# Performance work log

Measured on AMD Instinct MI355X. Metric: run time of the kernel, lower is better.

## Reference

```python
import jax, jax.numpy as jnp
import numpy as np

CHANNELS = 1024
N_HEADS = 16
N_EMBD = 512
H_DIM = CHANNELS // N_HEADS


def setup_inputs() -> dict:
    key = jax.random.key(0)
    ks = jax.random.split(key, 10)
    b, hw = 16, 4096
    s = 0.02
    return {
        "x": jax.random.normal(ks[0], (b, hw, CHANNELS), dtype=jnp.float32),
        "p": jax.random.normal(ks[1], (b, 77, N_EMBD), dtype=jnp.float32),
        "Wq": jax.random.normal(ks[2], (CHANNELS, CHANNELS), dtype=jnp.float32) * s,
        "bq": jnp.zeros((CHANNELS,), dtype=jnp.float32),
        "Wk": jax.random.normal(ks[3], (N_EMBD, CHANNELS), dtype=jnp.float32) * s,
        "bk": jnp.zeros((CHANNELS,), dtype=jnp.float32),
        "Wv": jax.random.normal(ks[4], (N_EMBD, CHANNELS), dtype=jnp.float32) * s,
        "bv": jnp.zeros((CHANNELS,), dtype=jnp.float32),
        "Ww": jax.random.normal(ks[5], (CHANNELS, CHANNELS), dtype=jnp.float32) * s,
        "bw": jnp.zeros((CHANNELS,), dtype=jnp.float32),
    }


def reference(x, p, Wq, bq, Wk, bk, Wv, bv, Ww, bw):
    b, hw, c = x.shape
    # Linear projections (torch Linear: y = x @ W^T + b; here weights stored as (in, out))
    q = x @ Wq + bq                      # (b, hw, c)
    k = p @ Wk + bk                      # (b, 77, c)
    v = p @ Wv + bv                      # (b, 77, c)
    q = q.reshape(b, hw, N_HEADS, H_DIM)
    k = k.reshape(b, 77, N_HEADS, H_DIM)
    v = v.reshape(b, 77, N_HEADS, H_DIM)
    scale = 1.0 / jnp.sqrt(jnp.asarray(H_DIM, dtype=x.dtype))
    # scores: (b, heads, hw, 77)
    scores = jnp.einsum("bqhd,bkhd->bhqk", q, k) * scale
    attn = jax.nn.softmax(scores, axis=-1)
    out = jnp.einsum("bhqk,bkhd->bqhd", attn, v).reshape(b, hw, c)
    return out @ Ww + bw
```

## Files before the change

kernel.cpp:

```cpp
#include <hip/hip_runtime.h>
#include <cstdint>
#include <type_traits>

typedef uint16_t u16;
typedef uint32_t u32;
typedef __attribute__((ext_vector_type(4))) float f32x4;
typedef __attribute__((ext_vector_type(8))) __bf16 vbf8;
typedef __attribute__((ext_vector_type(8))) short vs8;

template <typename T, typename = void>
struct CanMfma : std::false_type {};
template <typename T>
struct CanMfma<T, std::void_t<decltype(__builtin_amdgcn_mfma_f32_16x16x32_bf16(
    std::declval<T>(), std::declval<T>(), std::declval<f32x4>(), 0, 0, 0))>>
    : std::true_type {};
typedef std::conditional_t<CanMfma<vbf8>::value, vbf8, vs8> frag_t;

__device__ __forceinline__ f32x4 mfma_bf16(frag_t a, frag_t b, f32x4 c) {
  return __builtin_amdgcn_mfma_f32_16x16x32_bf16(a, b, c, 0, 0, 0);
}

__device__ __forceinline__ u16 f2bf(float f) {
  u32 u = __builtin_bit_cast(u32, f);
  u32 r = (u + 0x7FFFu + ((u >> 16) & 1u)) >> 16;
  return (u16)r;
}

__device__ __forceinline__ void gload_lds16(const void* g, void* l) {
  __builtin_amdgcn_global_load_lds(
      (const __attribute__((address_space(1))) void*)g,
      (__attribute__((address_space(3))) void*)l, 16, 0, 0);
}

__device__ __forceinline__ void transpose_body(
    const float* __restrict__ in, u16* __restrict__ out, int K, int N,
    int k0, int n0, float (*tile)[33]) {
  const int tr = threadIdx.x >> 5, tc = threadIdx.x & 31;
#pragma unroll
  for (int i = 0; i < 4; ++i)
    tile[tr + i * 8][tc] = in[(size_t)(k0 + tr + i * 8) * N + (n0 + tc)];
  __syncthreads();
#pragma unroll
  for (int i = 0; i < 4; ++i)
    out[(size_t)(n0 + tr + i * 8) * K + (k0 + tc)] = f2bf(tile[tc][tr + i * 8]);
}

__global__ __launch_bounds__(256) void prep_kernel(
    const float* __restrict__ x, const float* __restrict__ p,
    const float* __restrict__ Wq, const float* __restrict__ Ww,
    const float* __restrict__ Wk, const float* __restrict__ Wv,
    u16* __restrict__ x_bf, u16* __restrict__ p_bf,
    u16* __restrict__ wq_t, u16* __restrict__ ww_t, u16* __restrict__ wkv_t) {
  __shared__ float tile[32][33];
  const int bid = blockIdx.x;
  if (bid < 32768) {
    const size_t i = (size_t)bid * 256 + threadIdx.x;
    const float4 a  = ((const float4*)x)[i * 2];
    const float4 b2 = ((const float4*)x)[i * 2 + 1];
    uint4 o;
    o.x = (u32)f2bf(a.x)  | ((u32)f2bf(a.y)  << 16);
    o.y = (u32)f2bf(a.z)  | ((u32)f2bf(a.w)  << 16);
    o.z = (u32)f2bf(b2.x) | ((u32)f2bf(b2.y) << 16);
    o.w = (u32)f2bf(b2.z) | ((u32)f2bf(b2.w) << 16);
    ((uint4*)x_bf)[i] = o;
  } else if (bid < 33076) {
    const int i = (bid - 32768) * 256 + threadIdx.x;
    if (i < 78848) {
      const float4 a  = ((const float4*)p)[(size_t)i * 2];
      const float4 b2 = ((const float4*)p)[(size_t)i * 2 + 1];
      uint4 o;
      o.x = (u32)f2bf(a.x)  | ((u32)f2bf(a.y)  << 16);
      o.y = (u32)f2bf(a.z)  | ((u32)f2bf(a.w)  << 16);
      o.z = (u32)f2bf(b2.x) | ((u32)f2bf(b2.y) << 16);
      o.w = (u32)f2bf(b2.z) | ((u32)f2bf(b2.w) << 16);
      ((uint4*)p_bf)[(size_t)i] = o;
    }
  } else if (bid < 35124) {
    const bool isQ = bid < 34100;
    const int r = (bid - (isQ ? 33076 : 34100));
    transpose_body(isQ ? Wq : Ww, isQ ? wq_t : ww_t, 1024, 1024,
                   (r & 31) * 32, (r >> 5) * 32, tile);
  } else {
    const bool isK = bid < 35636;
    const int r = (bid - (isK ? 35124 : 35636));
    transpose_body(isK ? Wk : Wv, isK ? wkv_t : (wkv_t + 1024 * 512), 512, 1024,
                   (r & 15) * 32, (r >> 4) * 32, tile);
  }
}

template <bool OUT_BF16>
__global__ __launch_bounds__(256) void gemm_bt(
    const u16* __restrict__ A, const u16* __restrict__ Bt,
    const float* __restrict__ biasA, const float* __restrict__ biasB,
    void* __restrict__ Cout,
    int M, int N, int K, int Mtiles, int Ntiles) {
  __shared__ char Al[2][128 * 32 * 2];
  __shared__ char Bl[2][128 * 32 * 2];

  const int nwg = Mtiles * Ntiles;
  int bid = (int)blockIdx.x;
  bid = (bid & 7) * (nwg >> 3) + (bid >> 3);
  const int mt = bid / Ntiles, nt = bid % Ntiles;
  const int m0 = mt * 128, n0 = nt * 128;

  const int tid = (int)threadIdx.x;
  const int lane = tid & 63;
  const int wv = tid >> 6;
  const int wm = wv & 1, wn = wv >> 1;
  const int lr = lane & 15, lg = lane >> 4;
  const int rsub = lane >> 2;
  const int slot = lane & 3;
  const int rb0 = n0 + rsub;

  auto stage = [&](int buf, int t) {
    const int k0 = t << 5;
#pragma unroll
    for (int c = 0; c < 2; ++c) {
      const int ci = c * 4 + wv;
      int rra = m0 + ci * 16 + rsub;
      if (rra >= M) rra = M - 1;
      gload_lds16(A + (size_t)rra * K + k0 + slot * 8, Al[buf] + ci * 1024);
      const int rrb = rb0 + ci * 16;
      gload_lds16(Bt + (size_t)rrb * K + k0 + slot * 8, Bl[buf] + ci * 1024);
    }
  };

  f32x4 zero4 = {0.f, 0.f, 0.f, 0.f};
  f32x4 acc[4][4];
#pragma unroll
  for (int i = 0; i < 4; ++i)
#pragma unroll
    for (int j = 0; j < 4; ++j) acc[i][j] = zero4;

  const int nk = K >> 5;
  int cur = 0;
  stage(0, 0);
  __syncthreads();

  for (int t = 0; t < nk; ++t) {
    if (t + 1 < nk) stage(cur ^ 1, t + 1);
    frag_t af[4], bf[4];
#pragma unroll
    for (int i = 0; i < 4; ++i) {
      af[i] = *(const frag_t*)(Al[cur] + (wm * 64 + i * 16 + lr) * 64 + lg * 16);
      bf[i] = *(const frag_t*)(Bl[cur] + (wn * 64 + i * 16 + lr) * 64 + lg * 16);
    }
#pragma unroll
    for (int i = 0; i < 4; ++i)
#pragma unroll
      for (int j = 0; j < 4; ++j)
        acc[i][j] = mfma_bf16(af[i], bf[j], acc[i][j]);
    __syncthreads();
    cur ^= 1;
  }

#pragma unroll
  for (int j = 0; j < 4; ++j) {
    const int col = n0 + wn * 64 + j * 16 + lr;
    const float bv = (col < 1024) ? biasA[col] : biasB[col - 1024];
#pragma unroll
    for (int i = 0; i < 4; ++i) {
      const int rbase = m0 + wm * 64 + i * 16 + lg * 4;
#pragma unroll
      for (int r = 0; r < 4; ++r) {
        const int row = rbase + r;
        const float val = acc[i][j][r] + bv;
        if constexpr (OUT_BF16) {
          u32 me = f2bf(val);
          u32 other = __shfl_xor(me, 1);
          if ((lane & 1) == 0 && row < M) {
            *(u32*)((u16*)Cout + (size_t)row * N + col) = me | (other << 16);
          }
        } else {
          if (row < M) ((float*)Cout)[(size_t)row * N + col] = val;
        }
      }
    }
  }
}

template <bool OUT_BF16>
__global__ __launch_bounds__(512, 4) void gemm256(
    const u16* __restrict__ A, const u16* __restrict__ Bt,
    const float* __restrict__ bias, void* __restrict__ Cout,
    int M, int N, int K) {
  __shared__ u16 Al[2][256 * 32];
  __shared__ u16 Bl[2][128 * 32];

  const int Ntiles = N >> 7;
  const int nwg = (M >> 8) * Ntiles;
  int bid = (int)blockIdx.x;
  bid = (bid & 7) * (nwg >> 3) + (bid >> 3);
  const int mt = bid / Ntiles, ntl = bid % Ntiles;
  const int m0 = mt << 8, n0 = ntl << 7;

  const int tid = (int)threadIdx.x;
  const int lane = tid & 63;
  const int wid = tid >> 6;
  const int wm = wid >> 1, wn = wid & 1;
  const int lr = lane & 15, lg = lane >> 4;

  const int srow = lane >> 2;
  const int sslot = (lane & 3) ^ ((lane >> 3) & 3);
  const u16* Abase = A + (size_t)(m0 + wid * 32 + srow) * K + sslot * 8;
  const u16* Bbase = Bt + (size_t)(n0 + wid * 16 + srow) * K + sslot * 8;

  auto stage = [&](u16* da, u16* db, int t) {
    const int k0 = t << 5;
    gload_lds16(Abase + k0, (char*)da + wid * 2048);
    gload_lds16(Abase + ((size_t)K << 4) + k0, (char*)da + wid * 2048 + 1024);
    gload_lds16(Bbase + k0, (char*)db + wid * 1024);
  };

  auto ldsF = [&](const u16* base, int row) -> frag_t {
    const int phys = lg ^ ((row >> 1) & 3);
    return *(const frag_t*)(base + (size_t)row * 32 + phys * 8);
  };

  f32x4 zero4 = {0.f, 0.f, 0.f, 0.f};
  f32x4 acc[4][4];
#pragma unroll
  for (int i = 0; i < 4; ++i)
#pragma unroll
    for (int j = 0; j < 4; ++j) acc[i][j] = zero4;

  const int nt = K >> 5;
  const int ar0 = wm * 64 + lr;
  const int br0 = wn * 64 + lr;

  stage(&Al[0][0], &Bl[0][0], 0);
  stage(&Al[1][0], &Bl[1][0], 1);
  asm volatile("s_waitcnt vmcnt(3)" ::: "memory");
  __builtin_amdgcn_s_barrier();

  for (int t = 0; t < nt; ++t) {
    const int cur = t & 1;
    const u16* al = &Al[cur][0];
    const u16* bl = &Bl[cur][0];
    if (t >= 1 && t + 1 < nt)
      stage(&Al[cur ^ 1][0], &Bl[cur ^ 1][0], t + 1);
    frag_t a[4], b[4];
#pragma unroll
    for (int i = 0; i < 4; ++i) a[i] = ldsF(al, ar0 + i * 16);
#pragma unroll
    for (int j = 0; j < 4; ++j) b[j] = ldsF(bl, br0 + j * 16);
#pragma unroll
    for (int i = 0; i < 4; ++i)
#pragma unroll
      for (int j = 0; j < 4; ++j)
        acc[i][j] = mfma_bf16(a[i], b[j], acc[i][j]);
    if (t + 1 < nt) {
      asm volatile("s_waitcnt vmcnt(0)" ::: "memory");
      __builtin_amdgcn_s_barrier();
    }
  }

  float bvv[4];
#pragma unroll
  for (int bj = 0; bj < 4; ++bj) bvv[bj] = bias[n0 + wn * 64 + bj * 16 + lr];
#pragma unroll
  for (int ai = 0; ai < 4; ++ai) {
    const int rbase = m0 + wm * 64 + ai * 16 + lg * 4;
#pragma unroll
    for (int rr = 0; rr < 4; ++rr) {
      const int row = rbase + rr;
#pragma unroll
      for (int bj = 0; bj < 4; ++bj) {
        const int cb = n0 + wn * 64 + bj * 16;
        const float val = acc[ai][bj][rr] + bvv[bj];
        if constexpr (OUT_BF16) {
          u32 me = f2bf(val);
          u32 d0 = me | (__shfl_xor(me, 1) << 16);
          u32 d1 = __shfl_xor(d0, 2);
          if ((lane & 3) == 0) {
            uint2 o; o.x = d0; o.y = d1;
            *(uint2*)((u16*)Cout + (size_t)row * N + cb + (lr & 12)) = o;
          }
        } else {
          float v0 = val;
          float v1 = __shfl_xor(v0, 1);
          float v2 = __shfl_xor(v0, 2);
          float v3 = __shfl_xor(v1, 2);
          if ((lane & 3) == 0) {
            float4 o; o.x = v0; o.y = v1; o.z = v2; o.w = v3;
            *(float4*)((float*)Cout + (size_t)row * N + cb + (lr & 12)) = o;
          }
        }
      }
    }
  }
}

__global__ __launch_bounds__(256) void attn_kernel(
    const u16* __restrict__ Q, const u16* __restrict__ KV,
    u16* __restrict__ O) {
  __shared__ u16 Kl[96][72];
  __shared__ u16 Vt[64][104];

  const int bid = blockIdx.x;
  const int qt0 = bid & 15;
  const int h = (bid >> 4) & 15;
  const int b = bid >> 8;
  const int tid = threadIdx.x;

#pragma unroll
  for (int it = 0; it < 3; ++it) {
    const int idx = tid + it * 256;
    const int key = idx >> 3, s = idx & 7;
    uint4 val{0u, 0u, 0u, 0u};
    if (key < 77)
      val = *(const uint4*)(KV + ((size_t)(b * 77 + key)) * 2048 + h * 64 + s * 8);
    *(uint4*)(&Kl[key][s * 8]) = val;
  }
#pragma unroll
  for (int it = 0; it < 3; ++it) {
    const int idx = tid + it * 256;
    if (idx < 616) {
      const int key = idx >> 3, s = idx & 7;
      const uint4 v4 = *(const uint4*)(KV + ((size_t)(b * 77 + key)) * 2048 +
                                       1024 + h * 64 + s * 8);
      const u16* e = (const u16*)&v4;
#pragma unroll
      for (int j = 0; j < 8; ++j) Vt[s * 8 + j][key] = e[j];
    }
  }
#pragma unroll
  for (int it = 0; it < 5; ++it) {
    const int idx = tid + it * 256;
    if (idx < 1216) {
      const int d = idx / 19, kk = 77 + idx % 19;
      Vt[d][kk] = 0;
    }
  }
  __syncthreads();

  const int lane = tid & 63;
  const int wv = tid >> 6;
  const int lr = lane & 15;
  const int lg = lane >> 4;
  f32x4 zero4 = {0.f, 0.f, 0.f, 0.f};

  for (int q4 = 0; q4 < 4; ++q4) {
    const int qt = qt0 * 4 + q4;

    const size_t qrow = (size_t)(b * 4096 + qt * 64 + wv * 16 + lr) * 1024 + h * 64;
    frag_t qf[2];
#pragma unroll
    for (int ks = 0; ks < 2; ++ks)
      qf[ks] = *(const frag_t*)(Q + qrow + ks * 32 + lg * 8);

    f32x4 sa[5] = {zero4, zero4, zero4, zero4, zero4};
#pragma unroll
    for (int ks = 0; ks < 2; ++ks) {
#pragma unroll
      for (int kt = 0; kt < 5; ++kt) {
        frag_t kf = *(const frag_t*)(&Kl[kt * 16 + lr][ks * 32 + lg * 8]);
        sa[kt] = mfma_bf16(kf, qf[ks], sa[kt]);
      }
    }

    float p[5][4];
    float mx = -3.0e38f;
#pragma unroll
    for (int kt = 0; kt < 5; ++kt)
#pragma unroll
      for (int r = 0; r < 4; ++r) {
        const int key = kt * 16 + lg * 4 + r;
        float s = sa[kt][r] * 0.125f;
        if (key >= 77) s = -3.0e38f;
        p[kt][r] = s;
        mx = fmaxf(mx, s);
      }
    mx = fmaxf(mx, __shfl_xor(mx, 16));
    mx = fmaxf(mx, __shfl_xor(mx, 32));
    float sum = 0.f;
#pragma unroll
    for (int kt = 0; kt < 5; ++kt)
#pragma unroll
      for (int r = 0; r < 4; ++r) {
        const float e = __expf(p[kt][r] - mx);
        p[kt][r] = e;
        sum += e;
      }
    sum += __shfl_xor(sum, 16);
    sum += __shfl_xor(sum, 32);
    const float rden = 1.0f / sum;
#pragma unroll
    for (int kt = 0; kt < 5; ++kt)
#pragma unroll
      for (int r = 0; r < 4; ++r) p[kt][r] *= rden;

    union FP { frag_t v; u16 e[8]; };
    frag_t pa[3];
#pragma unroll
    for (int kb = 0; kb < 3; ++kb) {
      FP f;
#pragma unroll
      for (int j = 0; j < 8; ++j) {
        const int kt = 2 * kb + (j >> 2);
        f.e[j] = (kt < 5) ? f2bf(p[kt][j & 3]) : (u16)0;
      }
      pa[kb] = f.v;
    }

    f32x4 oa[4] = {zero4, zero4, zero4, zero4};
#pragma unroll
    for (int nt = 0; nt < 4; ++nt) {
      const int d = nt * 16 + lr;
#pragma unroll
      for (int kb = 0; kb < 3; ++kb) {
        const int key0 = kb * 32 + lg * 4;
        FP vb;
        *(uint2*)(&vb.e[0]) = *(const uint2*)(&Vt[d][key0]);
        *(uint2*)(&vb.e[4]) = *(const uint2*)(&Vt[d][key0 + 16]);
        oa[nt] = mfma_bf16(pa[kb], vb.v, oa[nt]);
      }
    }

#pragma unroll
    for (int nt = 0; nt < 4; ++nt)
#pragma unroll
      for (int r = 0; r < 4; ++r) {
        const int qr = wv * 16 + lg * 4 + r;
        u32 me = f2bf(oa[nt][r]);
        u32 other = __shfl_xor(me, 1);
        if ((lane & 1) == 0) {
          *(u32*)(O + ((size_t)(b * 4096 + qt * 64 + qr)) * 1024 + h * 64 +
                  nt * 16 + lr) = me | (other << 16);
        }
      }
  }
}

extern "C" void kernel_launch(void* const* d_in, const int* in_sizes, int n_in,
                              void* d_out, int out_size, void* d_ws, size_t ws_size,
                              hipStream_t stream) {
  const float* x  = (const float*)d_in[0];
  const float* p  = (const float*)d_in[1];
  const float* Wq = (const float*)d_in[2];
  const float* bq = (const float*)d_in[3];
  const float* Wk = (const float*)d_in[4];
  const float* bk = (const float*)d_in[5];
  const float* Wv = (const float*)d_in[6];
  const float* bv = (const float*)d_in[7];
  const float* Ww = (const float*)d_in[8];
  const float* bw = (const float*)d_in[9];

  char* ws = (char*)d_ws;
  if (ws_size < 281034752ULL) return;

  u16* x_bf  = (u16*)(ws + 0);
  u16* q_bf  = (u16*)(ws + 134217728);
  u16* wq_t  = (u16*)(ws + 268435456);
  u16* ww_t  = (u16*)(ws + 270532608);
  u16* wkv_t = (u16*)(ws + 272629760);
  u16* p_bf  = (u16*)(ws + 274726912);
  u16* kv_bf = (u16*)(ws + 275988480);

  prep_kernel<<<36148, 256, 0, stream>>>(x, p, Wq, Ww, Wk, Wv,
                                         x_bf, p_bf, wq_t, ww_t, wkv_t);
  gemm_bt<true><<<160, 256, 0, stream>>>(p_bf, wkv_t, bk, bv, kv_bf,
                                         1232, 2048, 512, 10, 16);
  gemm256<true><<<2048, 512, 0, stream>>>(x_bf, wq_t, bq, q_bf, 65536, 1024, 1024);
  attn_kernel<<<4096, 256, 0, stream>>>(q_bf, kv_bf, x_bf);
  gemm256<false><<<2048, 512, 0, stream>>>(x_bf, ww_t, bw, d_out, 65536, 1024, 1024);
}
```

Baseline: 589.3 us.

## Add 256x256-tile ping-pong pipelined GEMM for the Q projection

Adds a new gemm8p kernel using 256x256 output tiles with 8 waves, double-buffered LDS filled by direct global-to-LDS loads, and a fine-grained schedule. That schedule interleaves LDS fragment reads, next-tile staging and MFMA quarters, using barriers, sched_barrier and setprio. It replaces gemm256 only for the Q projection, halving the grid to 1024 blocks. The aim is to hide global and LDS latency behind MFMA work and raise data reuse per tile. The trade-off is high register pressure from 128 accumulators at one block per CU, plus reliance on hand-tuned waitcnt counts.

```diff
diff --git a/kernel.cpp b/kernel.cpp
--- a/kernel.cpp
+++ b/kernel.cpp
@@ -31,6 +31,8 @@
       (const __attribute__((address_space(1))) void*)g,
       (__attribute__((address_space(3))) void*)l, 16, 0, 0);
 }
+
+#define SB0() __builtin_amdgcn_sched_barrier(0)
 
 __device__ __forceinline__ void transpose_body(
     const float* __restrict__ in, u16* __restrict__ out, int K, int N,
@@ -291,6 +293,183 @@
   }
 }
 
+template <bool OUT_BF16>
+__global__ __launch_bounds__(512, 1) void gemm8p(
+    const u16* __restrict__ A, const u16* __restrict__ Bt,
+    const float* __restrict__ bias, void* __restrict__ Cout,
+    int M, int N, int K) {
+  __shared__ u16 Al[2][256 * 64];
+  __shared__ u16 Bl[2][256 * 64];
+
+  const int Ntiles = N >> 8;
+  const int nwg = (M >> 8) * Ntiles;
+  int bid = (int)blockIdx.x;
+  bid = (bid & 7) * (nwg >> 3) + (bid >> 3);
+  const int mt = bid / Ntiles, ntl = bid % Ntiles;
+  const int m0 = mt << 8, n0 = ntl << 8;
+
+  const int tid = (int)threadIdx.x;
+  const int lane = tid & 63;
+  const int wid = tid >> 6;
+  const int wm = wid >> 2, wn = wid & 3;
+  const int lr = lane & 15, lg = lane >> 4;
+  const int sslot = (lane & 7) ^ (lane >> 3);
+  const int lrow = lane >> 3;
+
+  auto stageA = [&](u16* dst, int half, int t) {
+#pragma unroll
+    for (int sub = 0; sub < 2; ++sub) {
+      const int s = half + sub * 2;
+      const u16* g = A + (size_t)(m0 + s * 64 + wid * 8 + lrow) * K + t * 64 + sslot * 8;
+      u16* l = dst + (s & 1) * 8192 + (s >> 1) * 4096 + wid * 512;
+      gload_lds16(g, l);
+    }
+  };
+  auto stageB = [&](u16* dst, int half, int t) {
+#pragma unroll
+    for (int sub = 0; sub < 2; ++sub) {
+      const int ub = wid * 16 + sub * 8;
+      const int r = n0 + (ub >> 5) * 64 + half * 32 + (ub & 31) + lrow;
+      const u16* g = Bt + (size_t)r * K + t * 64 + sslot * 8;
+      u16* l = dst + half * 8192 + ub * 64;
+      gload_lds16(g, l);
+    }
+  };
+
+  auto ldsA = [&](const u16* base, int r, int ks) -> frag_t {
+    const int off = ((r >> 6) & 1) * 8192 + (r >> 7) * 4096 + (r & 63) * 64 +
+                    ((((ks) << 2) + lg) ^ (r & 7)) * 8;
+    return *(const frag_t*)(base + off);
+  };
+  auto ldsB = [&](const u16* base, int r, int ks) -> frag_t {
+    const int off = ((r >> 5) & 1) * 8192 + (r >> 6) * 2048 + (r & 31) * 64 +
+                    ((((ks) << 2) + lg) ^ (r & 7)) * 8;
+    return *(const frag_t*)(base + off);
+  };
+
+  f32x4 acc[8][4];
+#pragma unroll
+  for (int i = 0; i < 8; ++i)
+#pragma unroll
+    for (int j = 0; j < 4; ++j)
+#pragma unroll
+      for (int r = 0; r < 4; ++r) acc[i][j][r] = 0.f;
+
+  frag_t aR[4][2], b0R[2][2], b1R[2][2];
+  auto mmq = [&](frag_t (&bb)[2][2], int mo, int no) {
+    __builtin_amdgcn_s_setprio(1);
+#pragma unroll
+    for (int i = 0; i < 4; ++i)
+#pragma unroll
+      for (int j = 0; j < 2; ++j) {
+        acc[mo + i][no + j] = mfma_bf16(aR[i][0], bb[j][0], acc[mo + i][no + j]);
+        acc[mo + i][no + j] = mfma_bf16(aR[i][1], bb[j][1], acc[mo + i][no + j]);
+      }
+    __builtin_amdgcn_s_setprio(0);
+  };
+
+  const int nt = K >> 6;
+  const int arow = wm * 128 + lr;
+  const int brow = wn * 64 + lr;
+
+  stageA(&Al[0][0], 0, 0); stageA(&Al[0][0], 1, 0);
+  stageB(&Bl[0][0], 0, 0); stageB(&Bl[0][0], 1, 0);
+  stageA(&Al[1][0], 0, 1);
+  stageB(&Bl[1][0], 0, 1); stageB(&Bl[1][0], 1, 1);
+  asm volatile("s_waitcnt vmcnt(6)" ::: "memory");
+  __builtin_amdgcn_s_barrier();
+
+  for (int t = 0; t < nt; ++t) {
+    const int cur = t & 1;
+    const u16* bA = &Al[cur][0];
+    const u16* bB = &Bl[cur][0];
+#pragma unroll
+    for (int i = 0; i < 4; ++i) {
+      aR[i][0] = ldsA(bA, arow + i * 16, 0);
+      aR[i][1] = ldsA(bA, arow + i * 16, 1);
+    }
+#pragma unroll
+    for (int j = 0; j < 2; ++j) {
+      b0R[j][0] = ldsB(bB, brow + j * 16, 0);
+      b0R[j][1] = ldsB(bB, brow + j * 16, 1);
+    }
+    if (t + 1 < nt) stageA(&Al[cur ^ 1][0], 1, t + 1);
+    asm volatile("s_waitcnt lgkmcnt(8)" ::: "memory");
+    SB0();
+    __builtin_amdgcn_s_barrier();
+    asm volatile("s_waitcnt lgkmcnt(0)" ::: "memory");
+    SB0();
+    mmq(b0R, 0, 0);
+    __builtin_amdgcn_s_barrier();
+#pragma unroll
+    for (int j = 0; j < 2; ++j) {
+      b1R[j][0] = ldsB(bB, brow + 32 + j * 16, 0);
+      b1R[j][1] = ldsB(bB, brow + 32 + j * 16, 1);
+    }
+    if (t + 2 < nt) stageA(&Al[cur][0], 0, t + 2);
+    SB0();
+    __builtin_amdgcn_s_barrier();
+    asm volatile("s_waitcnt lgkmcnt(0)" ::: "memory");
+    SB0();
+    mmq(b1R, 0, 2);
+    __builtin_amdgcn_s_barrier();
+#pragma unroll
+    for (int i = 0; i < 4; ++i) {
+      aR[i][0] = ldsA(bA, arow + 64 + i * 16, 0);
+      aR[i][1] = ldsA(bA, arow + 64 + i * 16, 1);
+    }
+    if (t + 2 < nt) stageB(&Bl[cur][0], 0, t + 2);
+    SB0();
+    __builtin_amdgcn_s_barrier();
+    asm volatile("s_waitcnt lgkmcnt(0)" ::: "memory");
+    SB0();
+    mmq(b1R, 4, 2);
+    __builtin_amdgcn_s_barrier();
+    if (t + 2 < nt) stageB(&Bl[cur][0], 1, t + 2);
+    mmq(b0R, 4, 0);
+    if (t + 2 < nt)
+      asm volatile("s_waitcnt vmcnt(6)" ::: "memory");
+    else if (t + 1 < nt)
+      asm volatile("s_waitcnt vmcnt(0)" ::: "memory");
+    if (t + 1 < nt) __builtin_amdgcn_s_barrier();
+  }
+
+  float bvv[4];
+#pragma unroll
+  for (int nf = 0; nf < 4; ++nf) bvv[nf] = bias[n0 + wn * 64 + nf * 16 + lr];
+#pragma unroll
+  for (int mf = 0; mf < 8; ++mf) {
+    const int rbase = m0 + wm * 128 + mf * 16 + lg * 4;
+#pragma unroll
+    for (int rr = 0; rr < 4; ++rr) {
+      const int row = rbase + rr;
+#pragma unroll
+      for (int nf = 0; nf < 4; ++nf) {
+        const int cb = n0 + wn * 64 + nf * 16;
+        const float val = acc[mf][nf][rr] + bvv[nf];
+        if constexpr (OUT_BF16) {
+          u32 me = f2bf(val);
+          u32 d0 = me | (__shfl_xor(me, 1) << 16);
+          u32 d1 = __shfl_xor(d0, 2);
+          if ((lane & 3) == 0) {
+            uint2 o; o.x = d0; o.y = d1;
+            *(uint2*)((u16*)Cout + (size_t)row * N + cb + (lr & 12)) = o;
+          }
+        } else {
+          float v0 = val;
+          float v1 = __shfl_xor(v0, 1);
+          float v2 = __shfl_xor(v0, 2);
+          float v3 = __shfl_xor(v1, 2);
+          if ((lane & 3) == 0) {
+            float4 o; o.x = v0; o.y = v1; o.z = v2; o.w = v3;
+            *(float4*)((float*)Cout + (size_t)row * N + cb + (lr & 12)) = o;
+          }
+        }
+      }
+    }
+  }
+}
+
 __global__ __launch_bounds__(256) void attn_kernel(
     const u16* __restrict__ Q, const u16* __restrict__ KV,
     u16* __restrict__ O) {
@@ -461,7 +640,7 @@
                                          x_bf, p_bf, wq_t, ww_t, wkv_t);
   gemm_bt<true><<<160, 256, 0, stream>>>(p_bf, wkv_t, bk, bv, kv_bf,
                                          1232, 2048, 512, 10, 16);
-  gemm256<true><<<2048, 512, 0, stream>>>(x_bf, wq_t, bq, q_bf, 65536, 1024, 1024);
+  gemm8p<true><<<1024, 512, 0, stream>>>(x_bf, wq_t, bq, q_bf, 65536, 1024, 1024);
   attn_kernel<<<4096, 256, 0, stream>>>(q_bf, kv_bf, x_bf);
   gemm256<false><<<2048, 512, 0, stream>>>(x_bf, ww_t, bw, d_out, 65536, 1024, 1024);
 }
```

New measurement: 553.4 us. 1.06x faster.
